# Kernel tuning notes

Measured on AMD Instinct MI355X. Metric: run time of the kernel, lower is better.

Reference implementation:

```python
import jax, jax.numpy as jnp
import numpy as np

NUM_KERNELS = 6
ALPHA = 0.5
DIL = 9
FEAT = 4
DELTA_V = 0.5
DELTA_D = 1.5
EMB_W = 0.25
MAX_LABELS = 16


def setup_inputs() -> dict:
    key = jax.random.key(0)
    k1, k2, k3, k4, k5 = jax.random.split(key, 5)
    B, H, W = 8, 640, 640
    pred = jax.random.normal(k1, (B, NUM_KERNELS + FEAT, H, W), dtype=jnp.float32)
    gt_text = (jax.random.uniform(k2, (B, 1, H, W)) < 0.3).astype(jnp.float32)
    gt_kernels = (jax.random.uniform(k3, (B, NUM_KERNELS - 1, H, W)) < 0.2).astype(jnp.float32)
    training_mask = (jax.random.uniform(k4, (B, 1, H, W)) > 0.05).astype(jnp.float32)
    gt_instance = jax.random.randint(k5, (B, H, W), 0, MAX_LABELS, dtype=jnp.int32)
    return {"pred": pred, "gt_text": gt_text, "gt_kernels": gt_kernels,
            "training_mask": training_mask, "gt_instance": gt_instance}


def _dice(inp, tgt, msk, eps=1e-6):
    # inp/tgt/msk: [N, HW]; returns mean over N of (1 - 2*I/U)
    inp = inp * msk
    tgt = tgt * msk
    inter = (inp * tgt).sum(1)
    union = (inp ** 2).sum(1) + (tgt ** 2).sum(1) + eps
    return (1.0 - 2.0 * inter / union).mean()


def _ohem(pred, gt, tm, ratio=3):
    # Vectorized OHEM: keep all positives + top-(3*n_pos) hardest negatives per sample.
    B = gt.shape[0]
    p = pred.reshape(B, -1)
    g = gt.reshape(B, -1)
    m = tm.reshape(B, -1)
    pos = (g > 0.5) & (m > 0.5)
    neg = (g <= 0.5) & (m > 0.5)
    n_pos = pos.sum(1)
    n_neg = jnp.minimum(ratio * n_pos, neg.sum(1))
    score = jnp.where(neg, p, -jnp.inf)
    # rank[i,j] = position of element j in descending order of score[i]
    rank = jnp.argsort(jnp.argsort(-score, axis=1), axis=1)
    mask = pos | (neg & (rank < n_neg[:, None]))
    return mask.astype(pred.dtype).reshape(gt.shape)


def _emb_sample(emb, gt, tm):
    # emb: [D,H,W], gt: [H,W] int, tm: [H,W]
    D = emb.shape[0]
    e = emb.reshape(D, -1).T                       # [HW, D]
    g = gt.reshape(-1)
    valid = tm.reshape(-1) > 0
    ids = jnp.where(valid, g, MAX_LABELS)          # invalid pixels -> dump segment
    ones = valid.astype(e.dtype)
    counts = jax.ops.segment_sum(ones, ids, num_segments=MAX_LABELS + 1)[:MAX_LABELS]
    sums = jax.ops.segment_sum(e * ones[:, None], ids, num_segments=MAX_LABELS + 1)[:MAX_LABELS]
    present = counts > 0
    n = present.sum()
    nf = n.astype(e.dtype)
    means = sums / jnp.maximum(counts, 1.0)[:, None]   # [L, D]
    # variance term: per-pixel distance to own cluster mean
    own = means[g]                                     # [HW, D]
    d = jnp.sqrt(((e - own) ** 2).sum(1) + 1e-12)
    cv = jnp.maximum(d - DELTA_V, 0.0) ** 2
    per = jax.ops.segment_sum(cv * ones, ids, num_segments=MAX_LABELS + 1)[:MAX_LABELS]
    per = per / jnp.maximum(counts, 1.0)
    lv = jnp.where(present, per, 0.0).sum() / jnp.maximum(nf, 1.0)
    # distance term: pairwise over present cluster means (unordered pairs i<j)
    diff = means[:, None, :] - means[None, :, :]
    pd = jnp.sqrt((diff ** 2).sum(-1) + 1e-12)
    iu = jnp.arange(MAX_LABELS)
    pm = present[:, None] & present[None, :] & (iu[:, None] < iu[None, :])
    ld = jnp.where(pm, jnp.maximum(2.0 * DELTA_D - pd, 0.0) ** 2, 0.0).sum()
    ld = ld / jnp.maximum(nf * (nf - 1.0), 1.0)
    # regularization: mean norm of present cluster means
    lr = jnp.where(present, jnp.sqrt((means ** 2).sum(1) + 1e-12), 0.0).sum() / jnp.maximum(nf, 1.0)
    act = (n > 1).astype(e.dtype)   # skip samples with <=1 instance (matches `continue`)
    return act * lv, act * ld, act * lr


def reference(pred, gt_text, gt_kernels, training_mask, gt_instance):
    B = pred.shape[0]
    gt_t = gt_text[:, 0]
    tm = training_mask[:, 0]
    # text branch: sigmoid -> 9x9 max-pool dilation -> OHEM dice
    prob = jax.nn.sigmoid(pred[:, 0])
    pad = DIL // 2
    dil = jax.lax.reduce_window(prob, -jnp.inf, jax.lax.max,
                                (1, DIL, DIL), (1, 1, 1),
                                [(0, 0), (pad, pad), (pad, pad)])
    ohem = jax.lax.stop_gradient(_ohem(dil, gt_t, tm, ratio=3))
    loss_text = _dice(dil.reshape(B, -1), gt_t.reshape(B, -1), ohem.reshape(B, -1))
    # kernel branch: mean over (B, K) equals sum_k dice_k / K
    K = NUM_KERNELS - 1
    pk = jax.nn.sigmoid(pred[:, 1:NUM_KERNELS]).reshape(B * K, -1)
    gk = gt_kernels.reshape(B * K, -1)
    mk = jnp.broadcast_to(tm[:, None], (B, K) + tm.shape[1:]).reshape(B * K, -1)
    loss_kernels = _dice(pk, gk, mk)
    # embedding clustering loss
    pred_emb = pred[:, NUM_KERNELS:]
    lv, ld, lr = jax.vmap(_emb_sample)(pred_emb, gt_instance, tm)
    loss_emb = EMB_W * (lv.sum() + ld.sum() + 0.001 * (lr.sum() / B))
    loss = loss_kernels + ALPHA * loss_text + loss_emb
    return loss, loss_text, loss_kernels, loss_emb
```

## Files before the change

kernel.cpp:

```cpp
#include <hip/hip_runtime.h>
#include <math.h>

#define BB 8
#define HH 640
#define WW 640
#define HWN (HH*WW)
#define CC 10
#define KCH 5
#define DD 4
#define LL 16
#define NBINS 256
#define ETILE 1024

#define WS_OHEM      0
#define WS_HCNT      64
#define WS_HS2       (WS_HCNT + BB*NBINS)
#define WS_KERN      (WS_HS2 + BB*NBINS)
#define WS_ECNT      (WS_KERN + 120)
#define WS_ESUM      (WS_ECNT + BB*LL)
#define WS_ECV       (WS_ESUM + BB*LL*DD)
#define WS_ZERO_END  (WS_ECV + BB)

typedef short bf16x8 __attribute__((ext_vector_type(8)));
typedef float f32x4  __attribute__((ext_vector_type(4)));

__device__ __forceinline__ float sigm(float x) { return 1.f / (1.f + __expf(-x)); }

__device__ __forceinline__ float wave_red(float v) {
    #pragma unroll
    for (int o = 32; o > 0; o >>= 1) v += __shfl_down(v, o);
    return v;
}

__device__ __forceinline__ unsigned short f2bf(float x) {
    return (unsigned short)((__float_as_uint(x) + 0x8000u) >> 16);
}

__device__ __forceinline__ float4 ld4g(const float* __restrict__ p, int row, int cb) {
    float4 v;
    if (row < 0 || row >= HH) { v.x = v.y = v.z = v.w = -INFINITY; return v; }
    const float* rp = p + (size_t)row * WW;
    if (cb >= 0 && cb <= WW - 4) return *(const float4*)(rp + cb);
    v.x = ((unsigned)(cb + 0) < (unsigned)WW) ? rp[cb + 0] : -INFINITY;
    v.y = ((unsigned)(cb + 1) < (unsigned)WW) ? rp[cb + 1] : -INFINITY;
    v.z = ((unsigned)(cb + 2) < (unsigned)WW) ? rp[cb + 2] : -INFINITY;
    v.w = ((unsigned)(cb + 3) < (unsigned)WW) ? rp[cb + 3] : -INFINITY;
    return v;
}

__global__ __launch_bounds__(256) void k_dil_stats(
    const float* __restrict__ pred, const float* __restrict__ gt_t,
    const float* __restrict__ tm, float* __restrict__ ws)
{
    __shared__ float hmax[72][65];
    __shared__ float hcnt[2][NBINS];
    __shared__ float hs2[2][NBINS];
    __shared__ float red[8];
    const int b  = blockIdx.z;
    const int x0 = blockIdx.x * 64;
    const int y0 = blockIdx.y * 64;
    const int tid = threadIdx.x;
    const float* p0 = pred + (size_t)b * CC * HWN;

    for (int i = tid; i < 2 * NBINS; i += 256) {
        ((float*)hcnt)[i] = 0.f; ((float*)hs2)[i] = 0.f;
    }
    if (tid < 8) red[tid] = 0.f;

    for (int i = tid; i < 72 * 16; i += 256) {
        int r = i >> 4, g = i & 15;
        int gr = y0 + r - 4;
        int cb = x0 + 4 * g - 4;
        float4 A  = ld4g(p0, gr, cb);
        float4 Bv = ld4g(p0, gr, cb + 4);
        float4 Cv = ld4g(p0, gr, cb + 8);
        float s3 = A.w;
        float s2 = fmaxf(A.z, s3);
        float s1 = fmaxf(A.y, s2);
        float s0 = fmaxf(A.x, s1);
        float mid = fmaxf(fmaxf(Bv.x, Bv.y), fmaxf(Bv.z, Bv.w));
        float q0 = Cv.x;
        float q1 = fmaxf(q0, Cv.y);
        float q2 = fmaxf(q1, Cv.z);
        float q3 = fmaxf(q2, Cv.w);
        int c = 4 * g;
        hmax[r][c + 0] = fmaxf(fmaxf(s0, mid), q0);
        hmax[r][c + 1] = fmaxf(fmaxf(s1, mid), q1);
        hmax[r][c + 2] = fmaxf(fmaxf(s2, mid), q2);
        hmax[r][c + 3] = fmaxf(fmaxf(s3, mid), q3);
    }
    __syncthreads();

    const int c  = tid & 63;
    const int rb = tid >> 6;
    const int hc = tid >> 7;
    float c_pos = 0.f, s_pos = 0.f, s_pos2 = 0.f, c_neg = 0.f, s_neg2 = 0.f;
    #pragma unroll
    for (int k = 0; k < 16; k++) {
        int r = rb * 16 + k;
        float m = hmax[r][c];
        #pragma unroll
        for (int j = 1; j < 9; j++) m = fmaxf(m, hmax[r + j][c]);
        float dil = sigm(m);
        size_t gidx = (size_t)b * HWN + (size_t)(y0 + r) * WW + (x0 + c);
        float g = gt_t[gidx], mv = tm[gidx];
        if (mv > 0.5f) {
            if (g > 0.5f) { c_pos += 1.f; s_pos += dil; s_pos2 += dil * dil; }
            else {
                c_neg += 1.f; s_neg2 += dil * dil;
                int bin = (int)((m + 8.f) * 16.f);
                bin = min(max(bin, 0), NBINS - 1);
                atomicAdd(&hcnt[hc][bin], 1.f);
                atomicAdd(&hs2[hc][bin], dil * dil);
            }
        }
    }
    c_pos = wave_red(c_pos); s_pos = wave_red(s_pos); s_pos2 = wave_red(s_pos2);
    c_neg = wave_red(c_neg); s_neg2 = wave_red(s_neg2);
    if ((tid & 63) == 0) {
        atomicAdd(&red[0], c_pos);  atomicAdd(&red[1], s_pos);
        atomicAdd(&red[2], s_pos2); atomicAdd(&red[3], c_neg);
        atomicAdd(&red[4], s_neg2);
    }
    __syncthreads();
    float* oh = ws + WS_OHEM + b * 8;
    if (tid < 5) atomicAdd(&oh[tid], red[tid]);
    float* gh_c = ws + WS_HCNT + b * NBINS;
    float* gh_s = ws + WS_HS2  + b * NBINS;
    for (int i = tid; i < NBINS; i += 256) {
        float sc = hcnt[0][i] + hcnt[1][i];
        if (sc != 0.f) {
            atomicAdd(&gh_c[i], sc);
            atomicAdd(&gh_s[i], hs2[0][i] + hs2[1][i]);
        }
    }
}

__global__ __launch_bounds__(256) void k_kern_dice(
    const float* __restrict__ pred, const float* __restrict__ gtk,
    const float* __restrict__ tm, float* __restrict__ ws)
{
    const int b = blockIdx.y;
    const float* pb = pred + ((size_t)b * CC + 1) * HWN;
    const float* gb = gtk + (size_t)b * KCH * HWN;
    const float4* m = (const float4*)(tm + (size_t)b * HWN);
    const int nv = HWN / 4;
    float i1[KCH], i2[KCH], i3[KCH];
    #pragma unroll
    for (int c = 0; c < KCH; c++) { i1[c] = 0.f; i2[c] = 0.f; i3[c] = 0.f; }

    for (int j = blockIdx.x * 256 + threadIdx.x; j < nv; j += gridDim.x * 256) {
        float4 mv = m[j];
        #pragma unroll
        for (int c = 0; c < KCH; c++) {
            float4 pv = ((const float4*)(pb + (size_t)c * HWN))[j];
            float4 gv = ((const float4*)(gb + (size_t)c * HWN))[j];
            float s0 = sigm(pv.x), s1 = sigm(pv.y), s2 = sigm(pv.z), s3 = sigm(pv.w);
            i1[c] += s0*gv.x*mv.x + s1*gv.y*mv.y + s2*gv.z*mv.z + s3*gv.w*mv.w;
            i2[c] += s0*s0*mv.x + s1*s1*mv.y + s2*s2*mv.z + s3*s3*mv.w;
            i3[c] += gv.x*mv.x + gv.y*mv.y + gv.z*mv.z + gv.w*mv.w;
        }
    }

    __shared__ float sred[4][15];
    const int wv = threadIdx.x >> 6;
    #pragma unroll
    for (int c = 0; c < KCH; c++) {
        float r1 = wave_red(i1[c]);
        float r2 = wave_red(i2[c]);
        float r3 = wave_red(i3[c]);
        if ((threadIdx.x & 63) == 0) {
            sred[wv][c*3+0] = r1; sred[wv][c*3+1] = r2; sred[wv][c*3+2] = r3;
        }
    }
    __syncthreads();
    if (threadIdx.x < 15) {
        float s = sred[0][threadIdx.x] + sred[1][threadIdx.x]
                + sred[2][threadIdx.x] + sred[3][threadIdx.x];
        int c = threadIdx.x / 3, jj = threadIdx.x - c * 3;
        atomicAdd(&ws[WS_KERN + (b * KCH + c) * 3 + jj], s);
    }
}

__global__ __launch_bounds__(256) void k_emb1(
    const float* __restrict__ pred, const int* __restrict__ inst,
    const float* __restrict__ tm, float* __restrict__ ws)
{
    const int b = blockIdx.y;
    __shared__ unsigned short chs[4][ETILE + 16];
    __shared__ unsigned int   labv[ETILE];
    __shared__ float          merge[4 * 80];
    const int tid  = threadIdx.x;
    const int wave = tid >> 6, lane = tid & 63;
    const int q = lane >> 4, n = lane & 15;
    const float* e0  = pred + ((size_t)b * CC + 6) * HWN;
    const float* tmb = tm + (size_t)b * HWN;
    const int*   ib  = inst + (size_t)b * HWN;

    const bool isch = (n >= 1 && n <= 4);
    const int  cn   = isch ? (n - 1) : 0;

    f32x4 acc = {0.f, 0.f, 0.f, 0.f};

    for (int t0 = blockIdx.x * ETILE; t0 < HWN; t0 += gridDim.x * ETILE) {
        {
            int p = t0 + tid * 4;
            float4 T = *(const float4*)(tmb + p);
            int4   L = *(const int4*)(ib + p);
            #pragma unroll
            for (int c = 0; c < 4; c++) {
                float4 V = *(const float4*)(e0 + (size_t)c * HWN + p);
                unsigned short* dst = &chs[c][tid * 4];
                dst[0] = f2bf(V.x); dst[1] = f2bf(V.y);
                dst[2] = f2bf(V.z); dst[3] = f2bf(V.w);
            }
            uint4 lv;
            lv.x = (T.x > 0.f) ? (unsigned)L.x : 255u;
            lv.y = (T.y > 0.f) ? (unsigned)L.y : 255u;
            lv.z = (T.z > 0.f) ? (unsigned)L.z : 255u;
            lv.w = (T.w > 0.f) ? (unsigned)L.w : 255u;
            *(uint4*)&labv[tid * 4] = lv;
        }
        __syncthreads();

        for (int c2 = wave; c2 < ETILE / 32; c2 += 4) {
            const int base = c2 * 32 + q * 8;
            uint4 La = *(const uint4*)&labv[base];
            uint4 Lb = *(const uint4*)&labv[base + 4];
            union { unsigned short u[8]; bf16x8 v; } A_;
            const unsigned un = (unsigned)n;
            A_.u[0] = (La.x == un) ? 0x3F80 : 0;
            A_.u[1] = (La.y == un) ? 0x3F80 : 0;
            A_.u[2] = (La.z == un) ? 0x3F80 : 0;
            A_.u[3] = (La.w == un) ? 0x3F80 : 0;
            A_.u[4] = (Lb.x == un) ? 0x3F80 : 0;
            A_.u[5] = (Lb.y == un) ? 0x3F80 : 0;
            A_.u[6] = (Lb.z == un) ? 0x3F80 : 0;
            A_.u[7] = (Lb.w == un) ? 0x3F80 : 0;
            bf16x8 Bf;
            if (isch) {
                Bf = *(const bf16x8*)&chs[cn][base];
            } else if (n == 0) {
                #pragma unroll
                for (int j = 0; j < 8; j++) Bf[j] = (short)0x3F80;
            } else {
                #pragma unroll
                for (int j = 0; j < 8; j++) Bf[j] = 0;
            }
            acc = __builtin_amdgcn_mfma_f32_16x16x32_bf16(A_.v, Bf, acc, 0, 0, 0);
        }
        __syncthreads();
    }

    if (n <= 4) {
        #pragma unroll
        for (int r = 0; r < 4; r++)
            merge[wave * 80 + (q * 4 + r) * 5 + n] = acc[r];
    }
    __syncthreads();
    if (tid < 80) {
        float s = merge[tid] + merge[80 + tid] + merge[160 + tid] + merge[240 + tid];
        int l = tid / 5, c = tid - l * 5;
        if (c == 0) atomicAdd(&ws[WS_ECNT + b * LL + l], s);
        else        atomicAdd(&ws[WS_ESUM + b * LL * DD + l * DD + (c - 1)], s);
    }
}

__global__ __launch_bounds__(256) void k_emb2(
    const float* __restrict__ pred, const int* __restrict__ inst,
    const float* __restrict__ tm, float* __restrict__ ws)
{
    const int b = blockIdx.y;
    const int tid = threadIdx.x;
    __shared__ float mn[LL * DD];
    __shared__ float invc[LL];
    if (tid < LL) {
        float c = ws[WS_ECNT + b * LL + tid];
        invc[tid] = 1.f / fmaxf(c, 1.f);
    }
    __syncthreads();
    if (tid < LL * DD) {
        int l = tid >> 2;
        mn[tid] = ws[WS_ESUM + b * LL * DD + tid] * invc[l];
    }
    __syncthreads();

    const float* e0 = pred + ((size_t)b * CC + 6) * HWN;
    const float4* v0p = (const float4*)e0;
    const float4* v1p = (const float4*)(e0 + HWN);
    const float4* v2p = (const float4*)(e0 + 2 * HWN);
    const float4* v3p = (const float4*)(e0 + 3 * HWN);
    const float4* tmv = (const float4*)(tm + (size_t)b * HWN);
    const int4*   iv  = (const int4*)(inst + (size_t)b * HWN);

    float acc = 0.f;
    const int nv = HWN / 4;
    for (int j = blockIdx.x * 256 + tid; j < nv; j += gridDim.x * 256) {
        float4 a0 = v0p[j], a1 = v1p[j], a2 = v2p[j], a3 = v3p[j];
        float4 t = tmv[j];
        int4 li = iv[j];
        float ex[4] = {a0.x, a0.y, a0.z, a0.w};
        float ey[4] = {a1.x, a1.y, a1.z, a1.w};
        float ez[4] = {a2.x, a2.y, a2.z, a2.w};
        float ew[4] = {a3.x, a3.y, a3.z, a3.w};
        int   lb[4] = {li.x, li.y, li.z, li.w};
        float tv[4] = {t.x, t.y, t.z, t.w};
        #pragma unroll
        for (int qq = 0; qq < 4; qq++) {
            int l = lb[qq];
            float d0 = ex[qq] - mn[l * DD + 0];
            float d1 = ey[qq] - mn[l * DD + 1];
            float d2 = ez[qq] - mn[l * DD + 2];
            float d3 = ew[qq] - mn[l * DD + 3];
            float dd = sqrtf(d0*d0 + d1*d1 + d2*d2 + d3*d3 + 1e-12f);
            float tt = fmaxf(dd - 0.5f, 0.f);
            float w = (tv[qq] > 0.f) ? invc[l] : 0.f;
            acc += w * tt * tt;
        }
    }

    acc = wave_red(acc);
    __shared__ float sred[4];
    const int wv = tid >> 6;
    if ((tid & 63) == 0) sred[wv] = acc;
    __syncthreads();
    if (tid == 0)
        atomicAdd(&ws[WS_ECV + b], sred[0] + sred[1] + sred[2] + sred[3]);
}

__global__ __launch_bounds__(256) void k_final(const float* __restrict__ ws, float* __restrict__ out)
{
    __shared__ float mn[BB][LL][DD];
    __shared__ float pres[BB][LL];
    __shared__ float nfa[BB], lda[BB], lra[BB];
    __shared__ float s_text[BB];
    __shared__ float s_kern[40];
    __shared__ float s_lv[BB], s_ld[BB], s_lr[BB];
    const int tid = threadIdx.x;
    if (tid < BB) { nfa[tid] = 0.f; lda[tid] = 0.f; lra[tid] = 0.f; }
    __syncthreads();
    if (tid < BB * LL) {
        int b = tid >> 4, l = tid & 15;
        float c = ws[WS_ECNT + b * LL + l];
        float inv = 1.f / fmaxf(c, 1.f);
        #pragma unroll
        for (int d = 0; d < DD; d++)
            mn[b][l][d] = ws[WS_ESUM + b * LL * DD + l * DD + d] * inv;
        float p = (c > 0.f) ? 1.f : 0.f;
        pres[b][l] = p;
        atomicAdd(&nfa[b], p);
    }
    __syncthreads();
    for (int t = tid; t < BB * 120; t += 256) {
        int b = t / 120, idx = t - b * 120, ii = 0;
        while (idx >= (LL - 1 - ii)) { idx -= (LL - 1 - ii); ii++; }
        int jj = ii + 1 + idx;
        if (pres[b][ii] > 0.f && pres[b][jj] > 0.f) {
            float s = 1e-12f;
            #pragma unroll
            for (int d = 0; d < DD; d++) {
                float df = mn[b][ii][d] - mn[b][jj][d]; s += df * df;
            }
            float tt = fmaxf(3.0f - sqrtf(s), 0.f);
            if (tt > 0.f) atomicAdd(&lda[b], tt * tt);
        }
    }
    if (tid < BB * LL) {
        int b = tid >> 4, l = tid & 15;
        if (pres[b][l] > 0.f) {
            float s = 1e-12f;
            #pragma unroll
            for (int d = 0; d < DD; d++) s += mn[b][l][d] * mn[b][l][d];
            atomicAdd(&lra[b], sqrtf(s));
        }
    }
    __syncthreads();
    if (tid < BB) {
        const float* o = ws + WS_OHEM + tid * 8;
        float npos = o[0], spos = o[1], spos2 = o[2], nnegt = o[3], sneg2t = o[4];
        float nneg = fminf(3.f * npos, nnegt);
        float ssel;
        if (nneg >= nnegt) ssel = sneg2t;
        else {
            const float* hcn = ws + WS_HCNT + tid * NBINS;
            const float* hs = ws + WS_HS2  + tid * NBINS;
            float acc = 0.f; ssel = 0.f;
            for (int i = NBINS - 1; i >= 0; i--) {
                float c = hcn[i];
                if (c <= 0.f) continue;
                if (acc + c <= nneg) { ssel += hs[i]; acc += c; }
                else { float r = nneg - acc; ssel += r * (hs[i] / c); break; }
            }
        }
        float uni = spos2 + ssel + npos + 1e-6f;
        s_text[tid] = 1.f - 2.f * spos / uni;

        float nf  = nfa[tid];
        float act = (nf > 1.f) ? 1.f : 0.f;
        s_lv[tid] = act * ws[WS_ECV + tid] / fmaxf(nf, 1.f);
        s_ld[tid] = act * lda[tid] / fmaxf(nf * (nf - 1.f), 1.f);
        s_lr[tid] = act * lra[tid] / fmaxf(nf, 1.f);
    }
    if (tid < 40) {
        const float* kk = ws + WS_KERN + tid * 3;
        s_kern[tid] = 1.f - 2.f * kk[0] / (kk[1] + kk[2] + 1e-6f);
    }
    __syncthreads();
    if (tid == 0) {
        float lt = 0.f; for (int i = 0; i < BB; i++) lt += s_text[i]; lt /= (float)BB;
        float lk = 0.f; for (int i = 0; i < 40; i++) lk += s_kern[i]; lk /= 40.f;
        float lvs = 0.f, lds_ = 0.f, lrs = 0.f;
        for (int i = 0; i < BB; i++) { lvs += s_lv[i]; lds_ += s_ld[i]; lrs += s_lr[i]; }
        float lemb = 0.25f * (lvs + lds_ + 0.001f * (lrs / (float)BB));
        out[0] = lk + 0.5f * lt + lemb;
        out[1] = lt;
        out[2] = lk;
        out[3] = lemb;
    }
}

extern "C" void kernel_launch(void* const* d_in, const int* in_sizes, int n_in,
                              void* d_out, int out_size, void* d_ws, size_t ws_size,
                              hipStream_t stream)
{
    (void)in_sizes; (void)n_in; (void)out_size; (void)ws_size;
    const float* pred = (const float*)d_in[0];
    const float* gt_t = (const float*)d_in[1];
    const float* gtk  = (const float*)d_in[2];
    const float* tm   = (const float*)d_in[3];
    const int*   inst = (const int*)d_in[4];
    float* out = (float*)d_out;
    float* ws  = (float*)d_ws;

    hipMemsetAsync(d_ws, 0, WS_ZERO_END * sizeof(float), stream);

    dim3 g1(WW / 64, HH / 64, BB), b1(256, 1, 1);
    k_dil_stats<<<g1, b1, 0, stream>>>(pred, gt_t, tm, ws);
    k_kern_dice<<<dim3(96, BB), 256, 0, stream>>>(pred, gtk, tm, ws);
    k_emb1<<<dim3(64, BB), 256, 0, stream>>>(pred, inst, tm, ws);
    k_emb2<<<dim3(128, BB), 256, 0, stream>>>(pred, inst, tm, ws);
    k_final<<<1, 256, 0, stream>>>(ws, out);
}
```

Baseline: 333.5 us.

## Merge dilation and kernel-dice into one launch; fuse embedding passes via grid barrier

Combines the text-dilation stats kernel and the kernel-branch dice kernel into one heterogeneous launch, with the block index selecting the role, so both run concurrently and fill the device. The two embedding passes become one kernel that uses a software grid-wide barrier (atomic counter plus spin) between the mean accumulation and the variance pass. The dice part now uses 256 blocks per batch instead of 96. This removes launch gaps and tail underutilisation. The grid barrier assumes all 512 embedding blocks are co-resident; it adds spin overhead and could deadlock if they are not.

```diff
diff --git a/kernel.cpp b/kernel.cpp
--- a/kernel.cpp
+++ b/kernel.cpp
@@ -12,6 +12,11 @@
 #define NBINS 256
 #define ETILE 1024
 
+#define NDIL   800
+#define NDICEB 2048
+#define EGX    64
+#define EGRID  (EGX * BB)
+
 #define WS_OHEM      0
 #define WS_HCNT      64
 #define WS_HS2       (WS_HCNT + BB*NBINS)
@@ -19,7 +24,8 @@
 #define WS_ECNT      (WS_KERN + 120)
 #define WS_ESUM      (WS_ECNT + BB*LL)
 #define WS_ECV       (WS_ESUM + BB*LL*DD)
-#define WS_ZERO_END  (WS_ECV + BB)
+#define WS_BAR       (WS_ECV + BB)
+#define WS_ZERO_END  (WS_BAR + 4)
 
 typedef short bf16x8 __attribute__((ext_vector_type(8)));
 typedef float f32x4  __attribute__((ext_vector_type(4)));
@@ -48,141 +54,142 @@
     return v;
 }
 
-__global__ __launch_bounds__(256) void k_dil_stats(
+__global__ __launch_bounds__(256) void k_front(
     const float* __restrict__ pred, const float* __restrict__ gt_t,
-    const float* __restrict__ tm, float* __restrict__ ws)
+    const float* __restrict__ gtk,  const float* __restrict__ tm,
+    float* __restrict__ ws)
 {
-    __shared__ float hmax[72][65];
-    __shared__ float hcnt[2][NBINS];
-    __shared__ float hs2[2][NBINS];
-    __shared__ float red[8];
-    const int b  = blockIdx.z;
-    const int x0 = blockIdx.x * 64;
-    const int y0 = blockIdx.y * 64;
+    __shared__ float smem[72 * 65 + 4 * NBINS + 8];
     const int tid = threadIdx.x;
-    const float* p0 = pred + (size_t)b * CC * HWN;
-
-    for (int i = tid; i < 2 * NBINS; i += 256) {
-        ((float*)hcnt)[i] = 0.f; ((float*)hs2)[i] = 0.f;
-    }
-    if (tid < 8) red[tid] = 0.f;
-
-    for (int i = tid; i < 72 * 16; i += 256) {
-        int r = i >> 4, g = i & 15;
-        int gr = y0 + r - 4;
-        int cb = x0 + 4 * g - 4;
-        float4 A  = ld4g(p0, gr, cb);
-        float4 Bv = ld4g(p0, gr, cb + 4);
-        float4 Cv = ld4g(p0, gr, cb + 8);
-        float s3 = A.w;
-        float s2 = fmaxf(A.z, s3);
-        float s1 = fmaxf(A.y, s2);
-        float s0 = fmaxf(A.x, s1);
-        float mid = fmaxf(fmaxf(Bv.x, Bv.y), fmaxf(Bv.z, Bv.w));
-        float q0 = Cv.x;
-        float q1 = fmaxf(q0, Cv.y);
-        float q2 = fmaxf(q1, Cv.z);
-        float q3 = fmaxf(q2, Cv.w);
-        int c = 4 * g;
-        hmax[r][c + 0] = fmaxf(fmaxf(s0, mid), q0);
-        hmax[r][c + 1] = fmaxf(fmaxf(s1, mid), q1);
-        hmax[r][c + 2] = fmaxf(fmaxf(s2, mid), q2);
-        hmax[r][c + 3] = fmaxf(fmaxf(s3, mid), q3);
-    }
-    __syncthreads();
-
-    const int c  = tid & 63;
-    const int rb = tid >> 6;
-    const int hc = tid >> 7;
-    float c_pos = 0.f, s_pos = 0.f, s_pos2 = 0.f, c_neg = 0.f, s_neg2 = 0.f;
-    #pragma unroll
-    for (int k = 0; k < 16; k++) {
-        int r = rb * 16 + k;
-        float m = hmax[r][c];
-        #pragma unroll
-        for (int j = 1; j < 9; j++) m = fmaxf(m, hmax[r + j][c]);
-        float dil = sigm(m);
-        size_t gidx = (size_t)b * HWN + (size_t)(y0 + r) * WW + (x0 + c);
-        float g = gt_t[gidx], mv = tm[gidx];
-        if (mv > 0.5f) {
-            if (g > 0.5f) { c_pos += 1.f; s_pos += dil; s_pos2 += dil * dil; }
-            else {
-                c_neg += 1.f; s_neg2 += dil * dil;
-                int bin = (int)((m + 8.f) * 16.f);
-                bin = min(max(bin, 0), NBINS - 1);
-                atomicAdd(&hcnt[hc][bin], 1.f);
-                atomicAdd(&hs2[hc][bin], dil * dil);
-            }
-        }
-    }
-    c_pos = wave_red(c_pos); s_pos = wave_red(s_pos); s_pos2 = wave_red(s_pos2);
-    c_neg = wave_red(c_neg); s_neg2 = wave_red(s_neg2);
-    if ((tid & 63) == 0) {
-        atomicAdd(&red[0], c_pos);  atomicAdd(&red[1], s_pos);
-        atomicAdd(&red[2], s_pos2); atomicAdd(&red[3], c_neg);
-        atomicAdd(&red[4], s_neg2);
-    }
-    __syncthreads();
-    float* oh = ws + WS_OHEM + b * 8;
-    if (tid < 5) atomicAdd(&oh[tid], red[tid]);
-    float* gh_c = ws + WS_HCNT + b * NBINS;
-    float* gh_s = ws + WS_HS2  + b * NBINS;
-    for (int i = tid; i < NBINS; i += 256) {
-        float sc = hcnt[0][i] + hcnt[1][i];
-        if (sc != 0.f) {
-            atomicAdd(&gh_c[i], sc);
-            atomicAdd(&gh_s[i], hs2[0][i] + hs2[1][i]);
-        }
-    }
-}
-
-__global__ __launch_bounds__(256) void k_kern_dice(
-    const float* __restrict__ pred, const float* __restrict__ gtk,
-    const float* __restrict__ tm, float* __restrict__ ws)
-{
-    const int b = blockIdx.y;
-    const float* pb = pred + ((size_t)b * CC + 1) * HWN;
-    const float* gb = gtk + (size_t)b * KCH * HWN;
-    const float4* m = (const float4*)(tm + (size_t)b * HWN);
-    const int nv = HWN / 4;
-    float i1[KCH], i2[KCH], i3[KCH];
-    #pragma unroll
-    for (int c = 0; c < KCH; c++) { i1[c] = 0.f; i2[c] = 0.f; i3[c] = 0.f; }
-
-    for (int j = blockIdx.x * 256 + threadIdx.x; j < nv; j += gridDim.x * 256) {
-        float4 mv = m[j];
+    const int blk = blockIdx.x;
+
+    if (blk < NDIL) {
+        float* hmax = smem;
+        float* hcnt = smem + 72 * 65;
+        float* hs2  = hcnt + 2 * NBINS;
+        float* red  = hs2 + 2 * NBINS;
+        const int b   = blk / 100;
+        const int rem = blk - b * 100;
+        const int y0  = (rem / 10) * 64;
+        const int x0  = (rem - (rem / 10) * 10) * 64;
+        const float* p0 = pred + (size_t)b * CC * HWN;
+
+        for (int i = tid; i < 4 * NBINS; i += 256) hcnt[i] = 0.f;
+        if (tid < 8) red[tid] = 0.f;
+
+        for (int i = tid; i < 72 * 16; i += 256) {
+            int r = i >> 4, g = i & 15;
+            int gr = y0 + r - 4;
+            int cb = x0 + 4 * g - 4;
+            float4 A  = ld4g(p0, gr, cb);
+            float4 Bv = ld4g(p0, gr, cb + 4);
+            float4 Cv = ld4g(p0, gr, cb + 8);
+            float s3 = A.w;
+            float s2 = fmaxf(A.z, s3);
+            float s1 = fmaxf(A.y, s2);
+            float s0 = fmaxf(A.x, s1);
+            float mid = fmaxf(fmaxf(Bv.x, Bv.y), fmaxf(Bv.z, Bv.w));
+            float q0 = Cv.x;
+            float q1 = fmaxf(q0, Cv.y);
+            float q2 = fmaxf(q1, Cv.z);
+            float q3 = fmaxf(q2, Cv.w);
+            int c = 4 * g;
+            hmax[r * 65 + c + 0] = fmaxf(fmaxf(s0, mid), q0);
+            hmax[r * 65 + c + 1] = fmaxf(fmaxf(s1, mid), q1);
+            hmax[r * 65 + c + 2] = fmaxf(fmaxf(s2, mid), q2);
+            hmax[r * 65 + c + 3] = fmaxf(fmaxf(s3, mid), q3);
+        }
+        __syncthreads();
+
+        const int c  = tid & 63;
+        const int rb = tid >> 6;
+        const int hc = (tid >> 7) * NBINS;
+        float c_pos = 0.f, s_pos = 0.f, s_pos2 = 0.f, c_neg = 0.f, s_neg2 = 0.f;
+        #pragma unroll
+        for (int k = 0; k < 16; k++) {
+            int r = rb * 16 + k;
+            float m = hmax[r * 65 + c];
+            #pragma unroll
+            for (int j = 1; j < 9; j++) m = fmaxf(m, hmax[(r + j) * 65 + c]);
+            float dil = sigm(m);
+            size_t gidx = (size_t)b * HWN + (size_t)(y0 + r) * WW + (x0 + c);
+            float g = gt_t[gidx], mv = tm[gidx];
+            if (mv > 0.5f) {
+                if (g > 0.5f) { c_pos += 1.f; s_pos += dil; s_pos2 += dil * dil; }
+                else {
+                    c_neg += 1.f; s_neg2 += dil * dil;
+                    int bin = (int)((m + 8.f) * 16.f);
+                    bin = min(max(bin, 0), NBINS - 1);
+                    atomicAdd(&hcnt[hc + bin], 1.f);
+                    atomicAdd(&hs2[hc + bin], dil * dil);
+                }
+            }
+        }
+        c_pos = wave_red(c_pos); s_pos = wave_red(s_pos); s_pos2 = wave_red(s_pos2);
+        c_neg = wave_red(c_neg); s_neg2 = wave_red(s_neg2);
+        if ((tid & 63) == 0) {
+            atomicAdd(&red[0], c_pos);  atomicAdd(&red[1], s_pos);
+            atomicAdd(&red[2], s_pos2); atomicAdd(&red[3], c_neg);
+            atomicAdd(&red[4], s_neg2);
+        }
+        __syncthreads();
+        float* oh = ws + WS_OHEM + b * 8;
+        if (tid < 5) atomicAdd(&oh[tid], red[tid]);
+        float* gh_c = ws + WS_HCNT + b * NBINS;
+        float* gh_s = ws + WS_HS2  + b * NBINS;
+        for (int i = tid; i < NBINS; i += 256) {
+            float sc = hcnt[i] + hcnt[NBINS + i];
+            if (sc != 0.f) {
+                atomicAdd(&gh_c[i], sc);
+                atomicAdd(&gh_s[i], hs2[i] + hs2[NBINS + i]);
+            }
+        }
+    } else {
+        const int d  = blk - NDIL;
+        const int b  = d >> 8;
+        const int xb = d & 255;
+        const float* pb = pred + ((size_t)b * CC + 1) * HWN;
+        const float* gb = gtk + (size_t)b * KCH * HWN;
+        const float4* m = (const float4*)(tm + (size_t)b * HWN);
+        const int nv = HWN / 4;
+        float i1[KCH], i2[KCH], i3[KCH];
+        #pragma unroll
+        for (int c = 0; c < KCH; c++) { i1[c] = 0.f; i2[c] = 0.f; i3[c] = 0.f; }
+
+        for (int j = xb * 256 + tid; j < nv; j += 256 * 256) {
+            float4 mv = m[j];
+            #pragma unroll
+            for (int c = 0; c < KCH; c++) {
+                float4 pv = ((const float4*)(pb + (size_t)c * HWN))[j];
+                float4 gv = ((const float4*)(gb + (size_t)c * HWN))[j];
+                float s0 = sigm(pv.x), s1 = sigm(pv.y), s2 = sigm(pv.z), s3 = sigm(pv.w);
+                i1[c] += s0*gv.x*mv.x + s1*gv.y*mv.y + s2*gv.z*mv.z + s3*gv.w*mv.w;
+                i2[c] += s0*s0*mv.x + s1*s1*mv.y + s2*s2*mv.z + s3*s3*mv.w;
+                i3[c] += gv.x*mv.x + gv.y*mv.y + gv.z*mv.z + gv.w*mv.w;
+            }
+        }
+
+        float* sred = smem;
+        const int wv = tid >> 6;
         #pragma unroll
         for (int c = 0; c < KCH; c++) {
-            float4 pv = ((const float4*)(pb + (size_t)c * HWN))[j];
-            float4 gv = ((const float4*)(gb + (size_t)c * HWN))[j];
-            float s0 = sigm(pv.x), s1 = sigm(pv.y), s2 = sigm(pv.z), s3 = sigm(pv.w);
-            i1[c] += s0*gv.x*mv.x + s1*gv.y*mv.y + s2*gv.z*mv.z + s3*gv.w*mv.w;
-            i2[c] += s0*s0*mv.x + s1*s1*mv.y + s2*s2*mv.z + s3*s3*mv.w;
-            i3[c] += gv.x*mv.x + gv.y*mv.y + gv.z*mv.z + gv.w*mv.w;
-        }
-    }
-
-    __shared__ float sred[4][15];
-    const int wv = threadIdx.x >> 6;
-    #pragma unroll
-    for (int c = 0; c < KCH; c++) {
-        float r1 = wave_red(i1[c]);
-        float r2 = wave_red(i2[c]);
-        float r3 = wave_red(i3[c]);
-        if ((threadIdx.x & 63) == 0) {
-            sred[wv][c*3+0] = r1; sred[wv][c*3+1] = r2; sred[wv][c*3+2] = r3;
-        }
-    }
-    __syncthreads();
-    if (threadIdx.x < 15) {
-        float s = sred[0][threadIdx.x] + sred[1][threadIdx.x]
-                + sred[2][threadIdx.x] + sred[3][threadIdx.x];
-        int c = threadIdx.x / 3, jj = threadIdx.x - c * 3;
-        atomicAdd(&ws[WS_KERN + (b * KCH + c) * 3 + jj], s);
-    }
-}
-
-__global__ __launch_bounds__(256) void k_emb1(
+            float r1 = wave_red(i1[c]);
+            float r2 = wave_red(i2[c]);
+            float r3 = wave_red(i3[c]);
+            if ((tid & 63) == 0) {
+                sred[wv*15 + c*3+0] = r1; sred[wv*15 + c*3+1] = r2; sred[wv*15 + c*3+2] = r3;
+            }
+        }
+        __syncthreads();
+        if (tid < 15) {
+            float s = sred[tid] + sred[15 + tid] + sred[30 + tid] + sred[45 + tid];
+            int c = tid / 3, jj = tid - c * 3;
+            atomicAdd(&ws[WS_KERN + (b * KCH + c) * 3 + jj], s);
+        }
+    }
+}
+
+__global__ __launch_bounds__(256, 3) void k_emb(
     const float* __restrict__ pred, const int* __restrict__ inst,
     const float* __restrict__ tm, float* __restrict__ ws)
 {
@@ -202,7 +209,7 @@
 
     f32x4 acc = {0.f, 0.f, 0.f, 0.f};
 
-    for (int t0 = blockIdx.x * ETILE; t0 < HWN; t0 += gridDim.x * ETILE) {
+    for (int t0 = blockIdx.x * ETILE; t0 < HWN; t0 += EGX * ETILE) {
         {
             int p = t0 + tid * 4;
             float4 T = *(const float4*)(tmb + p);
@@ -264,14 +271,18 @@
         if (c == 0) atomicAdd(&ws[WS_ECNT + b * LL + l], s);
         else        atomicAdd(&ws[WS_ESUM + b * LL * DD + l * DD + (c - 1)], s);
     }
-}
-
-__global__ __launch_bounds__(256) void k_emb2(
-    const float* __restrict__ pred, const int* __restrict__ inst,
-    const float* __restrict__ tm, float* __restrict__ ws)
-{
-    const int b = blockIdx.y;
-    const int tid = threadIdx.x;
+    __syncthreads();
+
+    int* bar = (int*)(ws + WS_BAR);
+    if (tid == 0) {
+        __threadfence();
+        __hip_atomic_fetch_add(bar, 1, __ATOMIC_ACQ_REL, __HIP_MEMORY_SCOPE_AGENT);
+        while (__hip_atomic_load(bar, __ATOMIC_ACQUIRE, __HIP_MEMORY_SCOPE_AGENT) < EGRID) {
+            __builtin_amdgcn_s_sleep(8);
+        }
+    }
+    __syncthreads();
+
     __shared__ float mn[LL * DD];
     __shared__ float invc[LL];
     if (tid < LL) {
@@ -285,17 +296,16 @@
     }
     __syncthreads();
 
-    const float* e0 = pred + ((size_t)b * CC + 6) * HWN;
     const float4* v0p = (const float4*)e0;
     const float4* v1p = (const float4*)(e0 + HWN);
     const float4* v2p = (const float4*)(e0 + 2 * HWN);
     const float4* v3p = (const float4*)(e0 + 3 * HWN);
-    const float4* tmv = (const float4*)(tm + (size_t)b * HWN);
-    const int4*   iv  = (const int4*)(inst + (size_t)b * HWN);
-
-    float acc = 0.f;
+    const float4* tmv = (const float4*)tmb;
+    const int4*   iv  = (const int4*)ib;
+
+    float vacc = 0.f;
     const int nv = HWN / 4;
-    for (int j = blockIdx.x * 256 + tid; j < nv; j += gridDim.x * 256) {
+    for (int j = blockIdx.x * 256 + tid; j < nv; j += EGX * 256) {
         float4 a0 = v0p[j], a1 = v1p[j], a2 = v2p[j], a3 = v3p[j];
         float4 t = tmv[j];
         int4 li = iv[j];
@@ -315,14 +325,13 @@
             float dd = sqrtf(d0*d0 + d1*d1 + d2*d2 + d3*d3 + 1e-12f);
             float tt = fmaxf(dd - 0.5f, 0.f);
             float w = (tv[qq] > 0.f) ? invc[l] : 0.f;
-            acc += w * tt * tt;
-        }
-    }
-
-    acc = wave_red(acc);
+            vacc += w * tt * tt;
+        }
+    }
+
+    vacc = wave_red(vacc);
     __shared__ float sred[4];
-    const int wv = tid >> 6;
-    if ((tid & 63) == 0) sred[wv] = acc;
+    if ((tid & 63) == 0) sred[wave] = vacc;
     __syncthreads();
     if (tid == 0)
         atomicAdd(&ws[WS_ECV + b], sred[0] + sred[1] + sred[2] + sred[3]);
@@ -434,10 +443,7 @@
 
     hipMemsetAsync(d_ws, 0, WS_ZERO_END * sizeof(float), stream);
 
-    dim3 g1(WW / 64, HH / 64, BB), b1(256, 1, 1);
-    k_dil_stats<<<g1, b1, 0, stream>>>(pred, gt_t, tm, ws);
-    k_kern_dice<<<dim3(96, BB), 256, 0, stream>>>(pred, gtk, tm, ws);
-    k_emb1<<<dim3(64, BB), 256, 0, stream>>>(pred, inst, tm, ws);
-    k_emb2<<<dim3(128, BB), 256, 0, stream>>>(pred, inst, tm, ws);
+    k_front<<<NDIL + NDICEB, 256, 0, stream>>>(pred, gt_t, gtk, tm, ws);
+    k_emb<<<dim3(EGX, BB), 256, 0, stream>>>(pred, inst, tm, ws);
     k_final<<<1, 256, 0, stream>>>(ws, out);
 }
```

Result: slower. 363.5 us (+9.0%).
